# Kernel optimization log

Hardware: AMD Instinct MI355X
Metric: run time of the kernel (lower is better)

The kernel has to match this reference:

```python
import jax, jax.numpy as jnp
import numpy as np

NUM_HEADS = 16
D_MODEL = 1024
D_K = D_MODEL // NUM_HEADS
B, S = 2, 2048


def setup_inputs() -> dict:
    key = jax.random.key(0)
    ks = jax.random.split(key, 10)
    q = jax.random.normal(ks[0], (B, S, D_MODEL), dtype=jnp.float32)
    k = jax.random.normal(ks[1], (B, S, D_MODEL), dtype=jnp.float32)
    v = jax.random.normal(ks[2], (B, S, D_MODEL), dtype=jnp.float32)
    # causal mask, 1 = keep, 0 = masked (masked_fill(mask==0, -1e9))
    mask = jnp.tril(jnp.ones((S, S), dtype=jnp.int32))[None, None, :, :]
    # Linear weights ~ N(0, 0.02); biases left at torch default-ish small uniform
    std = 0.02
    Wq = jax.random.normal(ks[3], (D_MODEL, D_MODEL), dtype=jnp.float32) * std
    Wk = jax.random.normal(ks[4], (D_MODEL, D_MODEL), dtype=jnp.float32) * std
    Wv = jax.random.normal(ks[5], (D_MODEL, D_MODEL), dtype=jnp.float32) * std
    bound = 1.0 / np.sqrt(D_MODEL)
    bq = jax.random.uniform(ks[6], (D_MODEL,), jnp.float32, -bound, bound)
    bk = jax.random.uniform(ks[7], (D_MODEL,), jnp.float32, -bound, bound)
    bv = jax.random.uniform(ks[8], (D_MODEL,), jnp.float32, -bound, bound)
    return {"q": q, "k": k, "v": v, "mask": mask,
            "Wq": Wq, "bq": bq, "Wk": Wk, "bk": bk, "Wv": Wv, "bv": bv}


def reference(q, k, v, mask, Wq, bq, Wk, bk, Wv, bv):
    # projections (torch Linear: x @ W.T + b), split heads -> [B, H, S, Dk]
    def proj(x, W, b):
        y = x @ W.T + b
        return y.reshape(B, S, NUM_HEADS, D_K).transpose(0, 2, 1, 3)

    qh, kh, vh = proj(q, Wq, bq), proj(k, Wk, bk), proj(v, Wv, bv)
    scores = jnp.einsum('bhqd,bhkd->bhqk', qh, kh) / jnp.sqrt(jnp.float32(D_K))
    scores = jnp.where(mask == 0, jnp.float32(-1e9), scores)
    p = jax.nn.softmax(scores, axis=-1)
    # dropout is identity in eval mode
    x = jnp.einsum('bhqk,bhkd->bhqd', p, vh)  # [B, H, S, Dk]
    return x.transpose(0, 2, 1, 3).reshape(B, S, D_MODEL)
```

## Files before the change

kernel.cpp:

```cpp
#include <hip/hip_runtime.h>

#define B_ 2
#define H_ 16
#define S_ 2048
#define DM 1024
#define DK 64
#define NX (4096 * 1024)
#define NW (1024 * 1024)

typedef unsigned short u16;
typedef __attribute__((ext_vector_type(8))) short bf16x8;
typedef __attribute__((ext_vector_type(8))) unsigned short u16x8;
typedef __attribute__((ext_vector_type(4))) unsigned short u16x4;
typedef __attribute__((ext_vector_type(4))) float f32x4;

__device__ inline u16 f2bf(float f) {
  union { float f; unsigned int u; } c; c.f = f;
  unsigned int u = c.u;
  u += 0x7fffu + ((u >> 16) & 1u);
  return (u16)(u >> 16);
}

__device__ inline u16x8 cvt8(const float* __restrict__ src) {
  const float4 a = *reinterpret_cast<const float4*>(src);
  const float4 b = *reinterpret_cast<const float4*>(src + 4);
  u16x8 r;
  r[0] = f2bf(a.x); r[1] = f2bf(a.y); r[2] = f2bf(a.z); r[3] = f2bf(a.w);
  r[4] = f2bf(b.x); r[5] = f2bf(b.y); r[6] = f2bf(b.z); r[7] = f2bf(b.w);
  return r;
}

__device__ inline void glds16(const u16* g, u16* l) {
  __builtin_amdgcn_global_load_lds(
      (const __attribute__((address_space(1))) unsigned int*)g,
      (__attribute__((address_space(3))) unsigned int*)l, 16, 0, 0);
}

__global__ __launch_bounds__(256) void cvt_kernel(
    const float* __restrict__ q, const float* __restrict__ k, const float* __restrict__ v,
    const float* __restrict__ Wq, const float* __restrict__ Wk, const float* __restrict__ Wv,
    u16* __restrict__ Xq, u16* __restrict__ Xk, u16* __restrict__ Xv,
    u16* __restrict__ Wqb, u16* __restrict__ Wkb, u16* __restrict__ Wvb)
{
  const int t = blockIdx.y;
  const float* src = (t == 0) ? q : (t == 1) ? k : (t == 2) ? v
                   : (t == 3) ? Wq : (t == 4) ? Wk : Wv;
  u16* dst = (t == 0) ? Xq : (t == 1) ? Xk : (t == 2) ? Xv
           : (t == 3) ? Wqb : (t == 4) ? Wkb : Wvb;
  const int n = (t < 3) ? NX : NW;
  const int idx = (blockIdx.x * 256 + threadIdx.x) * 8;
  if (idx >= n) return;
  *reinterpret_cast<u16x8*>(&dst[idx]) = cvt8(&src[idx]);
}

__global__ __launch_bounds__(256) void proj_kernel(
    const u16* __restrict__ Xq, const u16* __restrict__ Xk, const u16* __restrict__ Xv,
    const u16* __restrict__ Wqb, const u16* __restrict__ Wkb, const u16* __restrict__ Wvb,
    const float* __restrict__ bq, const float* __restrict__ bk, const float* __restrict__ bv,
    u16* __restrict__ Qh, u16* __restrict__ Kh, u16* __restrict__ Vh)
{
  const int z = blockIdx.z;
  const u16* X      = (z == 0) ? Xq : (z == 1) ? Xk : Xv;
  const u16* W      = (z == 0) ? Wqb : (z == 1) ? Wkb : Wvb;
  const float* bias = (z == 0) ? bq : (z == 1) ? bk : bv;
  u16* out          = (z == 0) ? Qh : (z == 1) ? Kh : Vh;
  const float scale = (z == 0) ? 0.125f : 1.0f;

  __shared__ __align__(16) u16 Xs[128 * 32];
  __shared__ __align__(16) u16 Ws[128 * 32];

  const int tid = threadIdx.x;
  const int lane = tid & 63;
  const int w = tid >> 6;
  const int wy = w >> 1, wx = w & 1;
  const int m0 = blockIdx.y * 128;
  const int n0 = blockIdx.x * 128;
  const int ml = lane & 15;
  const int qd = lane >> 4;

  f32x4 acc[4][4] = {};

  for (int kb = 0; kb < DM; kb += 32) {
    __syncthreads();
    #pragma unroll
    for (int p = 0; p < 2; ++p) {
      const int c = p * 4 + w;
      const int row = c * 16 + (lane >> 2);
      const int col = kb + (lane & 3) * 8;
      glds16(&X[(size_t)(m0 + row) * DM + col], &Xs[c * 512]);
      glds16(&W[(size_t)(n0 + row) * DM + col], &Ws[c * 512]);
    }
    __syncthreads();
    bf16x8 a[4], bfr[4];
    #pragma unroll
    for (int i = 0; i < 4; ++i)
      a[i] = *reinterpret_cast<const bf16x8*>(&Xs[(wy * 64 + i * 16 + ml) * 32 + qd * 8]);
    #pragma unroll
    for (int j = 0; j < 4; ++j)
      bfr[j] = *reinterpret_cast<const bf16x8*>(&Ws[(wx * 64 + j * 16 + ml) * 32 + qd * 8]);
    #pragma unroll
    for (int i = 0; i < 4; ++i)
      #pragma unroll
      for (int j = 0; j < 4; ++j)
        acc[i][j] = __builtin_amdgcn_mfma_f32_16x16x32_bf16(a[i], bfr[j], acc[i][j], 0, 0, 0);
  }

  #pragma unroll
  for (int j = 0; j < 4; ++j) {
    const int n = n0 + wx * 64 + j * 16 + ml;
    const float badd = bias[n];
    const int h = n >> 6, d = n & 63;
    #pragma unroll
    for (int i = 0; i < 4; ++i) {
      #pragma unroll
      for (int r = 0; r < 4; ++r) {
        const int m = m0 + wy * 64 + i * 16 + qd * 4 + r;
        const int bi = m >> 11, s = m & 2047;
        out[((bi * H_ + h) * S_ + s) * DK + d] = f2bf((acc[i][j][r] + badd) * scale);
      }
    }
  }
}

__global__ __launch_bounds__(256) void transpose_kernel(
    const u16* __restrict__ Vh, u16* __restrict__ Vt)
{
  __shared__ __align__(16) u16 T[64 * 72];
  const int t = threadIdx.x;
  const int st = blockIdx.x, bh = blockIdx.y;
  {
    const int r = t >> 2, c = (t & 3) * 16;
    const u16* src = &Vh[((size_t)bh * S_ + st * 64 + r) * DK + c];
    *reinterpret_cast<u16x8*>(&T[r * 72 + c])     = *reinterpret_cast<const u16x8*>(src);
    *reinterpret_cast<u16x8*>(&T[r * 72 + c + 8]) = *reinterpret_cast<const u16x8*>(src + 8);
  }
  __syncthreads();
  {
    const int d = t >> 2, s0 = (t & 3) * 16;
    u16x8 a, b;
    #pragma unroll
    for (int i = 0; i < 8; ++i) a[i] = T[(s0 + i) * 72 + d];
    #pragma unroll
    for (int i = 0; i < 8; ++i) b[i] = T[(s0 + 8 + i) * 72 + d];
    u16* dst = &Vt[((size_t)bh * DK + d) * S_ + st * 64 + s0];
    *reinterpret_cast<u16x8*>(dst)     = a;
    *reinterpret_cast<u16x8*>(dst + 8) = b;
  }
}

__global__ __launch_bounds__(256) void attn_kernel(
    const u16* __restrict__ Qh, const u16* __restrict__ Kh,
    const u16* __restrict__ Vt, float* __restrict__ out)
{
  __shared__ __align__(16) u16 Ks[64 * 72];
  __shared__ __align__(16) u16 Vs[64 * 72];
  __shared__ __align__(16) u16 Ps[4 * 16 * 72];

  const int tid  = threadIdx.x;
  const int lane = tid & 63;
  const int w    = tid >> 6;
  const int qt   = (gridDim.x - 1) - blockIdx.x;
  const int bh   = blockIdx.y;
  const int b    = bh >> 4, h = bh & 15;
  const int ml   = lane & 15, qd = lane >> 4;
  const int R0   = qt * 64 + w * 16;

  bf16x8 qa[2];
  #pragma unroll
  for (int ch = 0; ch < 2; ++ch)
    qa[ch] = *reinterpret_cast<const bf16x8*>(
        &Qh[((size_t)bh * S_ + R0 + ml) * DK + ch * 32 + qd * 8]);

  f32x4 oacc[4] = {};
  float l = 0.f;

  const u16* kbase = Kh + (size_t)bh * S_ * DK;
  const u16* vbase = Vt + (size_t)bh * DK * S_;
  u16* pw = &Ps[w * 16 * 72 + ml * 72];

  const int sr = tid >> 3;
  const int sc = (tid & 7) * 8;

  for (int t = 0; t <= qt; ++t) {
    __syncthreads();
    #pragma unroll
    for (int p = 0; p < 2; ++p) {
      const int r = sr + p * 32;
      *reinterpret_cast<float4*>(&Ks[r * 72 + sc]) =
          *reinterpret_cast<const float4*>(&kbase[(size_t)(t * 64 + r) * DK + sc]);
      *reinterpret_cast<float4*>(&Vs[r * 72 + sc]) =
          *reinterpret_cast<const float4*>(&vbase[(size_t)r * S_ + t * 64 + sc]);
    }
    __syncthreads();

    const bool diag = (t == qt);
    const int jmax = diag ? w : 3;

    f32x4 sfr[4];
    #pragma unroll
    for (int j = 0; j < 4; ++j) {
      if (j > jmax) break;
      f32x4 zz = {};
      #pragma unroll
      for (int ch = 0; ch < 2; ++ch) {
        bf16x8 kb = *reinterpret_cast<const bf16x8*>(&Ks[(j * 16 + ml) * 72 + ch * 32 + qd * 8]);
        zz = __builtin_amdgcn_mfma_f32_16x16x32_bf16(kb, qa[ch], zz, 0, 0, 0);
      }
      sfr[j] = zz;
    }

    if (diag) {
      #pragma unroll
      for (int r = 0; r < 4; ++r)
        if (qd * 4 + r > ml) sfr[jmax][r] = -1e30f;
    }

    #pragma unroll
    for (int j = 0; j < 4; ++j) {
      if (j <= jmax) {
        u16x4 pk;
        #pragma unroll
        for (int r = 0; r < 4; ++r) {
          const float e = __expf(sfr[j][r]);
          l += e;
          pk[r] = f2bf(e);
        }
        *reinterpret_cast<u16x4*>(&pw[j * 16 + qd * 4]) = pk;
      } else {
        *reinterpret_cast<u16x4*>(&pw[j * 16 + qd * 4]) = (u16x4){0, 0, 0, 0};
      }
    }

    const int chmax = (diag && w < 2) ? 0 : 1;
    #pragma unroll
    for (int ch = 0; ch < 2; ++ch) {
      if (ch > chmax) break;
      bf16x8 pa = *reinterpret_cast<const bf16x8*>(&Ps[w * 16 * 72 + ml * 72 + ch * 32 + qd * 8]);
      #pragma unroll
      for (int dj = 0; dj < 4; ++dj) {
        bf16x8 vb = *reinterpret_cast<const bf16x8*>(&Vs[(dj * 16 + ml) * 72 + ch * 32 + qd * 8]);
        oacc[dj] = __builtin_amdgcn_mfma_f32_16x16x32_bf16(pa, vb, oacc[dj], 0, 0, 0);
      }
    }
  }

  l += __shfl_xor(l, 16, 64);
  l += __shfl_xor(l, 32, 64);
  float lr[4];
  #pragma unroll
  for (int r = 0; r < 4; ++r) lr[r] = __shfl(l, qd * 4 + r, 64);
  #pragma unroll
  for (int dj = 0; dj < 4; ++dj)
    #pragma unroll
    for (int r = 0; r < 4; ++r) {
      const int srow = R0 + qd * 4 + r;
      out[(size_t)(b * S_ + srow) * DM + h * DK + dj * 16 + ml] = oacc[dj][r] / lr[r];
    }
}

extern "C" void kernel_launch(void* const* d_in, const int* in_sizes, int n_in,
                              void* d_out, int out_size, void* d_ws, size_t ws_size,
                              hipStream_t stream) {
  const float* q  = (const float*)d_in[0];
  const float* k  = (const float*)d_in[1];
  const float* v  = (const float*)d_in[2];
  const float* Wq = (const float*)d_in[4];
  const float* bq = (const float*)d_in[5];
  const float* Wk = (const float*)d_in[6];
  const float* bk = (const float*)d_in[7];
  const float* Wv = (const float*)d_in[8];
  const float* bv = (const float*)d_in[9];

  u16* Xq  = (u16*)d_ws;
  u16* Xk  = Xq + NX;
  u16* Xv  = Xk + NX;
  u16* Wqb = Xv + NX;
  u16* Wkb = Wqb + NW;
  u16* Wvb = Wkb + NW;
  u16* Qh  = Wvb + NW;
  u16* Kh  = Qh + NX;
  u16* Vh  = Kh + NX;
  u16* Vt  = Xq;

  cvt_kernel<<<dim3(NX / (256 * 8), 6), 256, 0, stream>>>(
      q, k, v, Wq, Wk, Wv, Xq, Xk, Xv, Wqb, Wkb, Wvb);
  proj_kernel<<<dim3(DM / 128, (B_ * S_) / 128, 3), 256, 0, stream>>>(
      Xq, Xk, Xv, Wqb, Wkb, Wvb, bq, bk, bv, Qh, Kh, Vh);
  transpose_kernel<<<dim3(S_ / 64, B_ * H_), 256, 0, stream>>>(Vh, Vt);
  attn_kernel<<<dim3(S_ / 64, B_ * H_), 256, 0, stream>>>(
      Qh, Kh, Vt, (float*)d_out);
}
```

Baseline: 234.5 us.

## Fuse V transpose into projection epilogue, prefetch K/V tiles, pack exp with perm

The projection kernel now writes V directly in transposed layout through an LDS staging buffer in its epilogue, which removes the separate transpose kernel launch and one round trip of V through global memory. The attention kernel prefetches the next K/V tile into registers while computing on the current one, so global load latency overlaps with the MFMA work. The softmax exponentials are packed to bf16 by truncation with a byte-permute, and the row sum is taken from those truncated values so it stays consistent with P. Costs: LDS in the projection kernel grows to about 36KB, register pressure rises, and truncation replaces round-to-nearest for P.

```diff
diff --git a/kernel.cpp b/kernel.cpp
--- a/kernel.cpp
+++ b/kernel.cpp
@@ -9,14 +9,15 @@
 #define NW (1024 * 1024)
 
 typedef unsigned short u16;
+typedef unsigned int u32;
 typedef __attribute__((ext_vector_type(8))) short bf16x8;
 typedef __attribute__((ext_vector_type(8))) unsigned short u16x8;
 typedef __attribute__((ext_vector_type(4))) unsigned short u16x4;
 typedef __attribute__((ext_vector_type(4))) float f32x4;
 
 __device__ inline u16 f2bf(float f) {
-  union { float f; unsigned int u; } c; c.f = f;
-  unsigned int u = c.u;
+  union { float f; u32 u; } c; c.f = f;
+  u32 u = c.u;
   u += 0x7fffu + ((u >> 16) & 1u);
   return (u16)(u >> 16);
 }
@@ -57,17 +58,17 @@
     const u16* __restrict__ Xq, const u16* __restrict__ Xk, const u16* __restrict__ Xv,
     const u16* __restrict__ Wqb, const u16* __restrict__ Wkb, const u16* __restrict__ Wvb,
     const float* __restrict__ bq, const float* __restrict__ bk, const float* __restrict__ bv,
-    u16* __restrict__ Qh, u16* __restrict__ Kh, u16* __restrict__ Vh)
+    u16* __restrict__ Qh, u16* __restrict__ Kh, u16* __restrict__ Vt)
 {
   const int z = blockIdx.z;
   const u16* X      = (z == 0) ? Xq : (z == 1) ? Xk : Xv;
   const u16* W      = (z == 0) ? Wqb : (z == 1) ? Wkb : Wvb;
   const float* bias = (z == 0) ? bq : (z == 1) ? bk : bv;
-  u16* out          = (z == 0) ? Qh : (z == 1) ? Kh : Vh;
   const float scale = (z == 0) ? 0.125f : 1.0f;
 
-  __shared__ __align__(16) u16 Xs[128 * 32];
-  __shared__ __align__(16) u16 Ws[128 * 32];
+  __shared__ __align__(16) u16 SMEM[18432];
+  u16* Xs = SMEM;
+  u16* Ws = SMEM + 4096;
 
   const int tid = threadIdx.x;
   const int lane = tid & 63;
@@ -105,46 +106,46 @@
         acc[i][j] = __builtin_amdgcn_mfma_f32_16x16x32_bf16(a[i], bfr[j], acc[i][j], 0, 0, 0);
   }
 
-  #pragma unroll
-  for (int j = 0; j < 4; ++j) {
-    const int n = n0 + wx * 64 + j * 16 + ml;
-    const float badd = bias[n];
-    const int h = n >> 6, d = n & 63;
-    #pragma unroll
-    for (int i = 0; i < 4; ++i) {
-      #pragma unroll
-      for (int r = 0; r < 4; ++r) {
-        const int m = m0 + wy * 64 + i * 16 + qd * 4 + r;
-        const int bi = m >> 11, s = m & 2047;
-        out[((bi * H_ + h) * S_ + s) * DK + d] = f2bf((acc[i][j][r] + badd) * scale);
-      }
-    }
-  }
-}
-
-__global__ __launch_bounds__(256) void transpose_kernel(
-    const u16* __restrict__ Vh, u16* __restrict__ Vt)
-{
-  __shared__ __align__(16) u16 T[64 * 72];
-  const int t = threadIdx.x;
-  const int st = blockIdx.x, bh = blockIdx.y;
-  {
-    const int r = t >> 2, c = (t & 3) * 16;
-    const u16* src = &Vh[((size_t)bh * S_ + st * 64 + r) * DK + c];
-    *reinterpret_cast<u16x8*>(&T[r * 72 + c])     = *reinterpret_cast<const u16x8*>(src);
-    *reinterpret_cast<u16x8*>(&T[r * 72 + c + 8]) = *reinterpret_cast<const u16x8*>(src + 8);
-  }
-  __syncthreads();
-  {
-    const int d = t >> 2, s0 = (t & 3) * 16;
-    u16x8 a, b;
-    #pragma unroll
-    for (int i = 0; i < 8; ++i) a[i] = T[(s0 + i) * 72 + d];
-    #pragma unroll
-    for (int i = 0; i < 8; ++i) b[i] = T[(s0 + 8 + i) * 72 + d];
-    u16* dst = &Vt[((size_t)bh * DK + d) * S_ + st * 64 + s0];
-    *reinterpret_cast<u16x8*>(dst)     = a;
-    *reinterpret_cast<u16x8*>(dst + 8) = b;
+  if (z != 2) {
+    u16* out = (z == 0) ? Qh : Kh;
+    #pragma unroll
+    for (int j = 0; j < 4; ++j) {
+      const int n = n0 + wx * 64 + j * 16 + ml;
+      const float badd = bias[n];
+      const int h = n >> 6, d = n & 63;
+      #pragma unroll
+      for (int i = 0; i < 4; ++i) {
+        #pragma unroll
+        for (int r = 0; r < 4; ++r) {
+          const int m = m0 + wy * 64 + i * 16 + qd * 4 + r;
+          const int bi = m >> 11, s = m & 2047;
+          out[((bi * H_ + h) * S_ + s) * DK + d] = f2bf((acc[i][j][r] + badd) * scale);
+        }
+      }
+    }
+  } else {
+    __syncthreads();
+    u16* Tw = &SMEM[w * (64 * 72)];
+    #pragma unroll
+    for (int j = 0; j < 4; ++j) {
+      const float badd = bias[n0 + wx * 64 + j * 16 + ml];
+      #pragma unroll
+      for (int i = 0; i < 4; ++i) {
+        u16x4 pk;
+        #pragma unroll
+        for (int r = 0; r < 4; ++r) pk[r] = f2bf(acc[i][j][r] + badd);
+        *reinterpret_cast<u16x4*>(&Tw[(j * 16 + ml) * 72 + i * 16 + qd * 4]) = pk;
+      }
+    }
+    __syncthreads();
+    const int h   = (n0 + wx * 64) >> 6;
+    const int bi  = m0 >> 11;
+    const int s0g = (m0 & 2047) + wy * 64;
+    u16* dst = &Vt[(((size_t)bi * H_ + h) * DK + lane) * S_ + s0g];
+    const u16* srow = &Tw[lane * 72];
+    #pragma unroll
+    for (int c = 0; c < 8; ++c)
+      *reinterpret_cast<u16x8*>(&dst[c * 8]) = *reinterpret_cast<const u16x8*>(&srow[c * 8]);
   }
 }
 
@@ -181,17 +182,26 @@
   const int sr = tid >> 3;
   const int sc = (tid & 7) * 8;
 
+  float4 kr0 = *reinterpret_cast<const float4*>(&kbase[(size_t)sr * DK + sc]);
+  float4 kr1 = *reinterpret_cast<const float4*>(&kbase[(size_t)(sr + 32) * DK + sc]);
+  float4 vr0 = *reinterpret_cast<const float4*>(&vbase[(size_t)sr * S_ + sc]);
+  float4 vr1 = *reinterpret_cast<const float4*>(&vbase[(size_t)(sr + 32) * S_ + sc]);
+
   for (int t = 0; t <= qt; ++t) {
     __syncthreads();
-    #pragma unroll
-    for (int p = 0; p < 2; ++p) {
-      const int r = sr + p * 32;
-      *reinterpret_cast<float4*>(&Ks[r * 72 + sc]) =
-          *reinterpret_cast<const float4*>(&kbase[(size_t)(t * 64 + r) * DK + sc]);
-      *reinterpret_cast<float4*>(&Vs[r * 72 + sc]) =
-          *reinterpret_cast<const float4*>(&vbase[(size_t)r * S_ + t * 64 + sc]);
-    }
-    __syncthreads();
+    *reinterpret_cast<float4*>(&Ks[sr * 72 + sc])        = kr0;
+    *reinterpret_cast<float4*>(&Ks[(sr + 32) * 72 + sc]) = kr1;
+    *reinterpret_cast<float4*>(&Vs[sr * 72 + sc])        = vr0;
+    *reinterpret_cast<float4*>(&Vs[(sr + 32) * 72 + sc]) = vr1;
+    __syncthreads();
+
+    if (t < qt) {
+      const int tn = t + 1;
+      kr0 = *reinterpret_cast<const float4*>(&kbase[(size_t)(tn * 64 + sr) * DK + sc]);
+      kr1 = *reinterpret_cast<const float4*>(&kbase[(size_t)(tn * 64 + sr + 32) * DK + sc]);
+      vr0 = *reinterpret_cast<const float4*>(&vbase[(size_t)sr * S_ + tn * 64 + sc]);
+      vr1 = *reinterpret_cast<const float4*>(&vbase[(size_t)(sr + 32) * S_ + tn * 64 + sc]);
+    }
 
     const bool diag = (t == qt);
     const int jmax = diag ? w : 3;
@@ -217,18 +227,19 @@
 
     #pragma unroll
     for (int j = 0; j < 4; ++j) {
+      u32 p0 = 0, p1 = 0;
       if (j <= jmax) {
-        u16x4 pk;
-        #pragma unroll
-        for (int r = 0; r < 4; ++r) {
-          const float e = __expf(sfr[j][r]);
-          l += e;
-          pk[r] = f2bf(e);
-        }
-        *reinterpret_cast<u16x4*>(&pw[j * 16 + qd * 4]) = pk;
-      } else {
-        *reinterpret_cast<u16x4*>(&pw[j * 16 + qd * 4]) = (u16x4){0, 0, 0, 0};
-      }
+        union { float f; u32 u; } e0, e1, e2, e3, a0, a1, a2, a3;
+        e0.f = __expf(sfr[j][0]); e1.f = __expf(sfr[j][1]);
+        e2.f = __expf(sfr[j][2]); e3.f = __expf(sfr[j][3]);
+        p0 = __builtin_amdgcn_perm(e1.u, e0.u, 0x07060302u);
+        p1 = __builtin_amdgcn_perm(e3.u, e2.u, 0x07060302u);
+        a0.u = p0 << 16; a1.u = p0 & 0xFFFF0000u;
+        a2.u = p1 << 16; a3.u = p1 & 0xFFFF0000u;
+        l += (a0.f + a1.f) + (a2.f + a3.f);
+      }
+      u32* pd = reinterpret_cast<u32*>(&pw[j * 16 + qd * 4]);
+      pd[0] = p0; pd[1] = p1;
     }
 
     const int chmax = (diag && w < 2) ? 0 : 1;
@@ -279,14 +290,12 @@
   u16* Wvb = Wkb + NW;
   u16* Qh  = Wvb + NW;
   u16* Kh  = Qh + NX;
-  u16* Vh  = Kh + NX;
-  u16* Vt  = Xq;
+  u16* Vt  = Kh + NX;
 
   cvt_kernel<<<dim3(NX / (256 * 8), 6), 256, 0, stream>>>(
       q, k, v, Wq, Wk, Wv, Xq, Xk, Xv, Wqb, Wkb, Wvb);
   proj_kernel<<<dim3(DM / 128, (B_ * S_) / 128, 3), 256, 0, stream>>>(
-      Xq, Xk, Xv, Wqb, Wkb, Wvb, bq, bk, bv, Qh, Kh, Vh);
-  transpose_kernel<<<dim3(S_ / 64, B_ * H_), 256, 0, stream>>>(Vh, Vt);
+      Xq, Xk, Xv, Wqb, Wkb, Wvb, bq, bk, bv, Qh, Kh, Vt);
   attn_kernel<<<dim3(S_ / 64, B_ * H_), 256, 0, stream>>>(
       Qh, Kh, Vt, (float*)d_out);
 }
```

Result: no change. 238.5 us (+1.7%).

## Pair near and far causal query tiles per block and load K/V directly

Applied to the files above, without the earlier changes.

Each attention block now processes two query tiles (p and 31-p) so every block does equal causal work, halving the grid to 16 x 32 blocks. K and V fragments are loaded straight from global memory into registers, shared by both tiles, replacing the shared-memory staging and its two barriers per iteration. The softmax denominator is now summed from the bf16-rounded probabilities, using a perm-based pack. This raises register pressure and depends on caches for the uncoalesced per-lane global loads, and fewer blocks may reduce occupancy.

```diff
diff --git a/kernel.cpp b/kernel.cpp
--- a/kernel.cpp
+++ b/kernel.cpp
@@ -9,14 +9,14 @@
 #define NW (1024 * 1024)
 
 typedef unsigned short u16;
+typedef unsigned int u32;
 typedef __attribute__((ext_vector_type(8))) short bf16x8;
 typedef __attribute__((ext_vector_type(8))) unsigned short u16x8;
-typedef __attribute__((ext_vector_type(4))) unsigned short u16x4;
 typedef __attribute__((ext_vector_type(4))) float f32x4;
 
 __device__ inline u16 f2bf(float f) {
-  union { float f; unsigned int u; } c; c.f = f;
-  unsigned int u = c.u;
+  union { float f; u32 u; } c; c.f = f;
+  u32 u = c.u;
   u += 0x7fffu + ((u >> 16) & 1u);
   return (u16)(u >> 16);
 }
@@ -152,110 +152,124 @@
     const u16* __restrict__ Qh, const u16* __restrict__ Kh,
     const u16* __restrict__ Vt, float* __restrict__ out)
 {
-  __shared__ __align__(16) u16 Ks[64 * 72];
-  __shared__ __align__(16) u16 Vs[64 * 72];
   __shared__ __align__(16) u16 Ps[4 * 16 * 72];
 
   const int tid  = threadIdx.x;
   const int lane = tid & 63;
   const int w    = tid >> 6;
-  const int qt   = (gridDim.x - 1) - blockIdx.x;
+  const int p    = blockIdx.x;
   const int bh   = blockIdx.y;
   const int b    = bh >> 4, h = bh & 15;
   const int ml   = lane & 15, qd = lane >> 4;
-  const int R0   = qt * 64 + w * 16;
-
-  bf16x8 qa[2];
+  const int qtn  = p, qtf = 31 - p;
+  const int R0n  = qtn * 64 + w * 16;
+  const int R0f  = qtf * 64 + w * 16;
+
+  const u16* qb     = Qh + (size_t)bh * S_ * DK;
+  const u16* kbase  = Kh + (size_t)bh * S_ * DK;
+  const u16* vtbase = Vt + (size_t)bh * DK * S_;
+
+  bf16x8 qa[2][2];
   #pragma unroll
-  for (int ch = 0; ch < 2; ++ch)
-    qa[ch] = *reinterpret_cast<const bf16x8*>(
-        &Qh[((size_t)bh * S_ + R0 + ml) * DK + ch * 32 + qd * 8]);
-
-  f32x4 oacc[4] = {};
-  float l = 0.f;
-
-  const u16* kbase = Kh + (size_t)bh * S_ * DK;
-  const u16* vbase = Vt + (size_t)bh * DK * S_;
+  for (int ch = 0; ch < 2; ++ch) {
+    qa[0][ch] = *reinterpret_cast<const bf16x8*>(&qb[(size_t)(R0n + ml) * DK + ch * 32 + qd * 8]);
+    qa[1][ch] = *reinterpret_cast<const bf16x8*>(&qb[(size_t)(R0f + ml) * DK + ch * 32 + qd * 8]);
+  }
+
+  f32x4 oacc[2][4] = {};
+  float lsum[2] = {0.f, 0.f};
   u16* pw = &Ps[w * 16 * 72 + ml * 72];
 
-  const int sr = tid >> 3;
-  const int sc = (tid & 7) * 8;
-
-  for (int t = 0; t <= qt; ++t) {
-    __syncthreads();
-    #pragma unroll
-    for (int p = 0; p < 2; ++p) {
-      const int r = sr + p * 32;
-      *reinterpret_cast<float4*>(&Ks[r * 72 + sc]) =
-          *reinterpret_cast<const float4*>(&kbase[(size_t)(t * 64 + r) * DK + sc]);
-      *reinterpret_cast<float4*>(&Vs[r * 72 + sc]) =
-          *reinterpret_cast<const float4*>(&vbase[(size_t)r * S_ + t * 64 + sc]);
+  for (int t = 0; t <= qtf; ++t) {
+    const bool df = (t == qtf);
+    const int jK  = df ? w : 3;
+    const int chV = (df && w < 2) ? 0 : 1;
+
+    bf16x8 ka[4][2];
+    #pragma unroll
+    for (int j = 0; j < 4; ++j) {
+      if (j > jK) break;
+      #pragma unroll
+      for (int ch = 0; ch < 2; ++ch)
+        ka[j][ch] = *reinterpret_cast<const bf16x8*>(
+            &kbase[(size_t)(t * 64 + j * 16 + ml) * DK + ch * 32 + qd * 8]);
     }
-    __syncthreads();
-
-    const bool diag = (t == qt);
-    const int jmax = diag ? w : 3;
-
-    f32x4 sfr[4];
-    #pragma unroll
-    for (int j = 0; j < 4; ++j) {
-      if (j > jmax) break;
-      f32x4 zz = {};
+    bf16x8 vb[2][4];
+    #pragma unroll
+    for (int ch = 0; ch < 2; ++ch) {
+      if (ch > chV) break;
+      #pragma unroll
+      for (int dj = 0; dj < 4; ++dj)
+        vb[ch][dj] = *reinterpret_cast<const bf16x8*>(
+            &vtbase[(size_t)(dj * 16 + ml) * S_ + t * 64 + ch * 32 + qd * 8]);
+    }
+
+    auto do_tile = [&](int mt, bool diag) {
+      const int jmax = diag ? w : 3;
+      f32x4 sfr[4];
+      #pragma unroll
+      for (int j = 0; j < 4; ++j) {
+        if (j > jmax) break;
+        f32x4 zz = {};
+        #pragma unroll
+        for (int ch = 0; ch < 2; ++ch)
+          zz = __builtin_amdgcn_mfma_f32_16x16x32_bf16(ka[j][ch], qa[mt][ch], zz, 0, 0, 0);
+        sfr[j] = zz;
+      }
+      if (diag) {
+        #pragma unroll
+        for (int r = 0; r < 4; ++r)
+          if (qd * 4 + r > ml) sfr[jmax][r] = -1e30f;
+      }
+      #pragma unroll
+      for (int j = 0; j < 4; ++j) {
+        u32 p0 = 0, p1 = 0;
+        if (j <= jmax) {
+          union { float f; u32 u; } e0, e1, e2, e3, a0, a1, a2, a3;
+          e0.f = __expf(sfr[j][0]); e1.f = __expf(sfr[j][1]);
+          e2.f = __expf(sfr[j][2]); e3.f = __expf(sfr[j][3]);
+          p0 = __builtin_amdgcn_perm(e1.u, e0.u, 0x07060302u);
+          p1 = __builtin_amdgcn_perm(e3.u, e2.u, 0x07060302u);
+          a0.u = p0 << 16; a1.u = p0 & 0xFFFF0000u;
+          a2.u = p1 << 16; a3.u = p1 & 0xFFFF0000u;
+          lsum[mt] += (a0.f + a1.f) + (a2.f + a3.f);
+        }
+        u32* pd = reinterpret_cast<u32*>(&pw[j * 16 + qd * 4]);
+        pd[0] = p0; pd[1] = p1;
+      }
+      const int chmax = (diag && w < 2) ? 0 : 1;
       #pragma unroll
       for (int ch = 0; ch < 2; ++ch) {
-        bf16x8 kb = *reinterpret_cast<const bf16x8*>(&Ks[(j * 16 + ml) * 72 + ch * 32 + qd * 8]);
-        zz = __builtin_amdgcn_mfma_f32_16x16x32_bf16(kb, qa[ch], zz, 0, 0, 0);
-      }
-      sfr[j] = zz;
-    }
-
-    if (diag) {
-      #pragma unroll
-      for (int r = 0; r < 4; ++r)
-        if (qd * 4 + r > ml) sfr[jmax][r] = -1e30f;
-    }
-
-    #pragma unroll
-    for (int j = 0; j < 4; ++j) {
-      if (j <= jmax) {
-        u16x4 pk;
+        if (ch > chmax) break;
+        bf16x8 pa = *reinterpret_cast<const bf16x8*>(
+            &Ps[w * 16 * 72 + ml * 72 + ch * 32 + qd * 8]);
         #pragma unroll
-        for (int r = 0; r < 4; ++r) {
-          const float e = __expf(sfr[j][r]);
-          l += e;
-          pk[r] = f2bf(e);
-        }
-        *reinterpret_cast<u16x4*>(&pw[j * 16 + qd * 4]) = pk;
-      } else {
-        *reinterpret_cast<u16x4*>(&pw[j * 16 + qd * 4]) = (u16x4){0, 0, 0, 0};
-      }
-    }
-
-    const int chmax = (diag && w < 2) ? 0 : 1;
-    #pragma unroll
-    for (int ch = 0; ch < 2; ++ch) {
-      if (ch > chmax) break;
-      bf16x8 pa = *reinterpret_cast<const bf16x8*>(&Ps[w * 16 * 72 + ml * 72 + ch * 32 + qd * 8]);
-      #pragma unroll
-      for (int dj = 0; dj < 4; ++dj) {
-        bf16x8 vb = *reinterpret_cast<const bf16x8*>(&Vs[(dj * 16 + ml) * 72 + ch * 32 + qd * 8]);
-        oacc[dj] = __builtin_amdgcn_mfma_f32_16x16x32_bf16(pa, vb, oacc[dj], 0, 0, 0);
-      }
-    }
-  }
-
-  l += __shfl_xor(l, 16, 64);
-  l += __shfl_xor(l, 32, 64);
-  float lr[4];
+        for (int dj = 0; dj < 4; ++dj)
+          oacc[mt][dj] = __builtin_amdgcn_mfma_f32_16x16x32_bf16(pa, vb[ch][dj], oacc[mt][dj], 0, 0, 0);
+      }
+    };
+
+    do_tile(1, df);
+    if (t <= qtn) do_tile(0, t == qtn);
+  }
+
   #pragma unroll
-  for (int r = 0; r < 4; ++r) lr[r] = __shfl(l, qd * 4 + r, 64);
-  #pragma unroll
-  for (int dj = 0; dj < 4; ++dj)
-    #pragma unroll
-    for (int r = 0; r < 4; ++r) {
-      const int srow = R0 + qd * 4 + r;
-      out[(size_t)(b * S_ + srow) * DM + h * DK + dj * 16 + ml] = oacc[dj][r] / lr[r];
-    }
+  for (int mt = 0; mt < 2; ++mt) {
+    float lm = lsum[mt];
+    lm += __shfl_xor(lm, 16, 64);
+    lm += __shfl_xor(lm, 32, 64);
+    float lr[4];
+    #pragma unroll
+    for (int r = 0; r < 4; ++r) lr[r] = __shfl(lm, qd * 4 + r, 64);
+    const int R0 = mt ? R0f : R0n;
+    #pragma unroll
+    for (int dj = 0; dj < 4; ++dj)
+      #pragma unroll
+      for (int r = 0; r < 4; ++r) {
+        const int srow = R0 + qd * 4 + r;
+        out[(size_t)(b * S_ + srow) * DM + h * DK + dj * 16 + ml] = oacc[mt][dj][r] / lr[r];
+      }
+  }
 }
 
 extern "C" void kernel_launch(void* const* d_in, const int* in_sizes, int n_in,
@@ -287,6 +301,6 @@
   proj_kernel<<<dim3(DM / 128, (B_ * S_) / 128, 3), 256, 0, stream>>>(
       Xq, Xk, Xv, Wqb, Wkb, Wvb, bq, bk, bv, Qh, Kh, Vh);
   transpose_kernel<<<dim3(S_ / 64, B_ * H_), 256, 0, stream>>>(Vh, Vt);
-  attn_kernel<<<dim3(S_ / 64, B_ * H_), 256, 0, stream>>>(
+  attn_kernel<<<dim3(16, B_ * H_), 256, 0, stream>>>(
       Qh, Kh, Vt, (float*)d_out);
 }
```

After: 279.0 us. +18.9%, slower.
